# Optimization experiments

Hardware: AMD Instinct MI355X
Metric: run time of the kernel (lower is better)

## Reference

```python
import jax, jax.numpy as jnp
import numpy as np

N_ROWS = 8192
INPUT_DIM = 4096
EMBED_DIM = INPUT_DIM // 4
OUTPUT_DIM = 4096
NN = 16  # Taylor matrix size
RMS_EPS = 1.1920928955078125e-07  # torch fp32 finfo eps (F.rms_norm default)


def setup_inputs() -> dict:
    key = jax.random.key(0)
    ks = jax.random.split(key, 7)
    def lin(kw, fan_in, fan_out):
        bound = 1.0 / np.sqrt(fan_in)
        kw1, kw2 = jax.random.split(kw)
        W = jax.random.uniform(kw1, (fan_in, fan_out), jnp.float32, -bound, bound)
        b = jax.random.uniform(kw2, (fan_out,), jnp.float32, -bound, bound)
        return W, b
    x = jax.random.normal(ks[0], (N_ROWS, INPUT_DIM), jnp.float32)
    W_u, b_u = lin(ks[1], INPUT_DIM, EMBED_DIM)
    W_t, b_t = lin(ks[2], EMBED_DIM, NN * NN)
    W_s, b_s = lin(ks[3], NN * NN, OUTPUT_DIM)
    return {"x": x, "W_u": W_u, "b_u": b_u, "W_t": W_t, "b_t": b_t,
            "W_s": W_s, "b_s": b_s}


def _taylor_expm(M):
    # res = I + sum_{k=1}^{15} M^k / k!   (sequential, matches torch loop)
    B = M.shape[0]
    eye = jnp.broadcast_to(jnp.eye(NN, dtype=M.dtype), (B, NN, NN))
    def step(carry, k):
        term, res = carry
        term = jnp.einsum('bij,bjk->bik', term, M) / k
        return (term, res + term), None
    ks = jnp.arange(1, NN, dtype=M.dtype)
    (_, res), _ = jax.lax.scan(step, (eye, eye), ks)
    return res


def reference(x, W_u, b_u, W_t, b_t, W_s, b_s):
    # RMS norm (no learned scale)
    ms = jnp.mean(jnp.square(x), axis=-1, keepdims=True)
    xn = x * jax.lax.rsqrt(ms + RMS_EPS)
    latent = xn @ W_u + b_u                     # [N, embed]
    flat_m = latent @ W_t + b_t                 # [N, 256]
    mask = jnp.triu(jnp.ones((NN, NN), x.dtype), k=1).reshape(-1)
    flat_m = flat_m * mask
    m = flat_m.reshape(-1, NN, NN)              # [N, 16, 16] strictly upper
    exp_m = _taylor_expm(m)
    flat_exp = exp_m.reshape(x.shape[0], -1)    # [N, 256]
    return flat_exp @ W_s + b_s                 # [N, output_dim]
```

## Files before the change

### kernel.cpp

```cpp
#include <hip/hip_runtime.h>
#include <stdint.h>

typedef unsigned short u16;
typedef unsigned int u32;

using bf16x8 = __attribute__((ext_vector_type(8))) short;
using f32x4  = __attribute__((ext_vector_type(4))) float;

__device__ __forceinline__ float bf2f(u16 u) {
  union { u32 u; float f; } v; v.u = ((u32)u) << 16; return v.f;
}
__device__ __forceinline__ u16 f2bf(float f) {
  union { float f; u32 u; } v; v.f = f;
  u32 r = v.u + 0x7fffu + ((v.u >> 16) & 1u);
  return (u16)(r >> 16);
}
__device__ __forceinline__ short f2bf_s(float f) { return (short)f2bf(f); }

__global__ __launch_bounds__(256) void transpose_f32_bf16(
    const float* __restrict__ in, u16* __restrict__ out, int R, int C) {
  __shared__ u16 tile[32][33];
  const int tx = threadIdx.x, ty = threadIdx.y;
  const int icol = blockIdx.x * 32 + tx;
  const int irow0 = blockIdx.y * 32;
  #pragma unroll
  for (int i = ty; i < 32; i += 8)
    tile[i][tx] = f2bf(in[(size_t)(irow0 + i) * C + icol]);
  __syncthreads();
  const int ocol = blockIdx.y * 32 + tx;
  const int orow0 = blockIdx.x * 32;
  #pragma unroll
  for (int i = ty; i < 32; i += 8)
    out[(size_t)(orow0 + i) * R + ocol] = tile[tx][i];
}

__global__ __launch_bounds__(256) void rms_convert(
    const float* __restrict__ x, float* __restrict__ s, u16* __restrict__ xb, int K) {
  const int row = blockIdx.x;
  const float4* p = (const float4*)(x + (size_t)row * K);
  ushort4* q = (ushort4*)(xb + (size_t)row * K);
  float sum = 0.f;
  const int nvec = K >> 2;
  for (int i = threadIdx.x; i < nvec; i += 256) {
    float4 v = p[i];
    sum += v.x * v.x + v.y * v.y + v.z * v.z + v.w * v.w;
    ushort4 o;
    o.x = f2bf(v.x); o.y = f2bf(v.y); o.z = f2bf(v.z); o.w = f2bf(v.w);
    q[i] = o;
  }
  #pragma unroll
  for (int off = 32; off > 0; off >>= 1) sum += __shfl_down(sum, off, 64);
  __shared__ float part[4];
  if ((threadIdx.x & 63) == 0) part[threadIdx.x >> 6] = sum;
  __syncthreads();
  if (threadIdx.x == 0) {
    float tot = part[0] + part[1] + part[2] + part[3];
    s[row] = rsqrtf(tot / (float)K + 1.1920928955078125e-07f);
  }
}

template <int EPI, bool OUTF32>
__global__ __launch_bounds__(256) void gemm_bt(
    const u16* __restrict__ A, const u16* __restrict__ BT,
    const float* __restrict__ bias, const float* __restrict__ rowscale,
    void* __restrict__ Cv, int M, int N, int K) {
  __shared__ u16 As[128 * 32];
  __shared__ u16 Bs[128 * 32];
  const int t = threadIdx.x;
  const int lane = t & 63;
  const int w = t >> 6;
  const int wm = (w >> 1) * 64;
  const int wn = (w & 1) * 64;
  const int quad = lane >> 4;
  const int lrow = lane & 15;
  const int m0 = blockIdx.y * 128;
  const int n0 = blockIdx.x * 128;

  f32x4 acc[4][4] = {};

  const int srow = t >> 2;
  const int scol = (t & 3) * 8;
  const size_t abase = (size_t)(m0 + srow) * K + scol;
  const size_t bbase = (size_t)(n0 + srow) * K + scol;
  u16* const as_lo = As + srow * 32 + scol;
  u16* const as_hi = As + (64 + srow) * 32 + scol;
  u16* const bs_lo = Bs + srow * 32 + scol;
  u16* const bs_hi = Bs + (64 + srow) * 32 + scol;

  for (int k0 = 0; k0 < K; k0 += 32) {
    const bf16x8 ra0 = *(const bf16x8*)(A + abase + k0);
    const bf16x8 ra1 = *(const bf16x8*)(A + abase + (size_t)64 * K + k0);
    const bf16x8 rb0 = *(const bf16x8*)(BT + bbase + k0);
    const bf16x8 rb1 = *(const bf16x8*)(BT + bbase + (size_t)64 * K + k0);
    __syncthreads();
    *(bf16x8*)as_lo = ra0;
    *(bf16x8*)as_hi = ra1;
    *(bf16x8*)bs_lo = rb0;
    *(bf16x8*)bs_hi = rb1;
    __syncthreads();

    bf16x8 af[4], bv[4];
    #pragma unroll
    for (int i = 0; i < 4; ++i)
      af[i] = *(const bf16x8*)(As + (wm + i * 16 + lrow) * 32 + quad * 8);
    #pragma unroll
    for (int j = 0; j < 4; ++j)
      bv[j] = *(const bf16x8*)(Bs + (wn + j * 16 + lrow) * 32 + quad * 8);
    #pragma unroll
    for (int i = 0; i < 4; ++i)
      #pragma unroll
      for (int j = 0; j < 4; ++j)
        acc[i][j] = __builtin_amdgcn_mfma_f32_16x16x32_bf16(af[i], bv[j], acc[i][j], 0, 0, 0);
  }

  #pragma unroll
  for (int i = 0; i < 4; ++i) {
    const int row0 = m0 + wm + i * 16 + quad * 4;
    float sc[4];
    if (EPI == 0) {
      #pragma unroll
      for (int r = 0; r < 4; ++r) sc[r] = rowscale[row0 + r];
    }
    #pragma unroll
    for (int j = 0; j < 4; ++j) {
      const int col = n0 + wn + j * 16 + lrow;
      const float bvs = bias[col];
      #pragma unroll
      for (int r = 0; r < 4; ++r) {
        float v = acc[i][j][r];
        if (EPI == 0) v = v * sc[r] + bvs;
        else v += bvs;
        if (EPI == 1) {
          const int cc = col & 255;
          if ((cc & 15) <= (cc >> 4)) v = 0.f;
        }
        const size_t idx = (size_t)(row0 + r) * N + col;
        if (OUTF32) ((float*)Cv)[idx] = v;
        else        ((u16*)Cv)[idx] = f2bf(v);
      }
    }
  }
}

__global__ __launch_bounds__(256) void expm_taylor(
    const u16* __restrict__ Mi, u16* __restrict__ Eo) {
  __shared__ u16 mbuf[4][256];
  __shared__ float stage[2][4][16][17];
  const int t = threadIdx.x;
  const int w = t >> 6;
  const int lane = t & 63;
  const int q = lane >> 4;
  const int c = lane & 15;
  const size_t row = (size_t)blockIdx.x * 4 + w;

  *(uint2*)&mbuf[w][lane * 4] = *(const uint2*)(Mi + row * 256 + lane * 4);
  __syncthreads();

  const u16* mb = mbuf[w];
  const bf16x8 z8 = {0, 0, 0, 0, 0, 0, 0, 0};
  bf16x8 afrM = z8;
  bf16x8 bfr  = z8;
  if (q < 2) {
    #pragma unroll
    for (int jj = 0; jj < 8; ++jj) {
      afrM[jj] = (short)mb[c * 16 + q * 8 + jj];
      bfr[jj]  = (short)mb[(q * 8 + jj) * 16 + c];
    }
  }
  float res[4];
  #pragma unroll
  for (int r = 0; r < 4; ++r) {
    const int rw = q * 4 + r;
    res[r] = (rw == c ? 1.f : 0.f) + bf2f(mb[rw * 16 + c]);
  }

  for (int k = 2; k <= 15; ++k) {
    const f32x4 z = {0.f, 0.f, 0.f, 0.f};
    f32x4 P = __builtin_amdgcn_mfma_f32_16x16x32_bf16(afrM, bfr, z, 0, 0, 0);
    const float inv = 1.0f / (float)k;
    float tv[4];
    #pragma unroll
    for (int r = 0; r < 4; ++r) { tv[r] = P[r] * inv; res[r] += tv[r]; }
    if (k < 15) {
      #pragma unroll
      for (int r = 0; r < 4; ++r) stage[k & 1][w][q * 4 + r][c] = tv[r];
      __syncthreads();
      bfr = z8;
      if (q < 2) {
        #pragma unroll
        for (int jj = 0; jj < 8; ++jj) bfr[jj] = f2bf_s(stage[k & 1][w][q * 8 + jj][c]);
      }
    }
  }
  #pragma unroll
  for (int r = 0; r < 4; ++r)
    Eo[row * 256 + (size_t)(q * 4 + r) * 16 + c] = f2bf(res[r]);
}

extern "C" void kernel_launch(void* const* d_in, const int* in_sizes, int n_in,
                              void* d_out, int out_size, void* d_ws, size_t ws_size,
                              hipStream_t stream) {
  (void)in_sizes; (void)n_in; (void)out_size; (void)ws_size;
  const float* x   = (const float*)d_in[0];
  const float* W_u = (const float*)d_in[1];
  const float* b_u = (const float*)d_in[2];
  const float* W_t = (const float*)d_in[3];
  const float* b_t = (const float*)d_in[4];
  const float* W_s = (const float*)d_in[5];
  const float* b_s = (const float*)d_in[6];
  float* out = (float*)d_out;

  u16* xb     = (u16*)d_out;
  u16* latent = xb + (size_t)8192 * 4096;
  u16* mmat   = latent + (size_t)8192 * 1024;

  char* ws = (char*)d_ws;
  size_t off = 0;
  float* sscale = (float*)(ws + off); off += (size_t)8192 * sizeof(float);
  u16* WuT  = (u16*)(ws + off); off += (size_t)1024 * 4096 * 2;
  u16* WtT  = (u16*)(ws + off); off += (size_t)256 * 1024 * 2;
  u16* WsT  = (u16*)(ws + off); off += (size_t)4096 * 256 * 2;
  u16* eexp = (u16*)(ws + off); off += (size_t)8192 * 256 * 2;

  const dim3 tb(32, 8);
  transpose_f32_bf16<<<dim3(1024 / 32, 4096 / 32), tb, 0, stream>>>(W_u, WuT, 4096, 1024);
  transpose_f32_bf16<<<dim3(256 / 32, 1024 / 32), tb, 0, stream>>>(W_t, WtT, 1024, 256);
  transpose_f32_bf16<<<dim3(4096 / 32, 256 / 32), tb, 0, stream>>>(W_s, WsT, 256, 4096);

  rms_convert<<<8192, 256, 0, stream>>>(x, sscale, xb, 4096);

  gemm_bt<0, false><<<dim3(1024 / 128, 8192 / 128), 256, 0, stream>>>(
      xb, WuT, b_u, sscale, latent, 8192, 1024, 4096);
  gemm_bt<1, false><<<dim3(256 / 128, 8192 / 128), 256, 0, stream>>>(
      latent, WtT, b_t, nullptr, mmat, 8192, 256, 1024);
  expm_taylor<<<8192 / 4, 256, 0, stream>>>(mmat, eexp);
  gemm_bt<2, true><<<dim3(4096 / 128, 8192 / 128), 256, 0, stream>>>(
      eexp, WsT, b_s, nullptr, out, 8192, 4096, 256);
}
```

Before: 435.6 us.

## Load GEMM tiles directly into LDS with global_load_lds and XOR swizzle

Replaces the register-staged global-to-LDS copy in the bf16 GEMM with direct global_load_lds DMA loads of 16 bytes per lane. Each thread fetches a permuted 8-element column group chosen so that the linear per-thread LDS placement ends up XOR-swizzled, and the fragment reads apply the matching swizzle to reduce LDS bank conflicts. The aim is to cut VGPR staging and instruction overhead in the main loop. There is still no double buffering, so global latency stays exposed between the barriers, and correctness depends on the intrinsic's per-lane LDS placement matching t*4.

```diff
diff --git a/kernel.cpp b/kernel.cpp
--- a/kernel.cpp
+++ b/kernel.cpp
@@ -6,6 +6,11 @@
 
 using bf16x8 = __attribute__((ext_vector_type(8))) short;
 using f32x4  = __attribute__((ext_vector_type(4))) float;
+
+#define GLOBAL_AS __attribute__((address_space(1)))
+#define LDS_AS    __attribute__((address_space(3)))
+
+#define SWZ(r) (((r) >> 1) & 3)
 
 __device__ __forceinline__ float bf2f(u16 u) {
   union { u32 u; float f; } v; v.u = ((u32)u) << 16; return v.f;
@@ -79,33 +84,30 @@
   f32x4 acc[4][4] = {};
 
   const int srow = t >> 2;
-  const int scol = (t & 3) * 8;
-  const size_t abase = (size_t)(m0 + srow) * K + scol;
-  const size_t bbase = (size_t)(n0 + srow) * K + scol;
-  u16* const as_lo = As + srow * 32 + scol;
-  u16* const as_hi = As + (64 + srow) * 32 + scol;
-  u16* const bs_lo = Bs + srow * 32 + scol;
-  u16* const bs_hi = Bs + (64 + srow) * 32 + scol;
+  const int sg   = (t & 3) ^ SWZ(srow);
+  const size_t abase = (size_t)(m0 + srow) * K + sg * 8;
+  const size_t bbase = (size_t)(n0 + srow) * K + sg * 8;
 
   for (int k0 = 0; k0 < K; k0 += 32) {
-    const bf16x8 ra0 = *(const bf16x8*)(A + abase + k0);
-    const bf16x8 ra1 = *(const bf16x8*)(A + abase + (size_t)64 * K + k0);
-    const bf16x8 rb0 = *(const bf16x8*)(BT + bbase + k0);
-    const bf16x8 rb1 = *(const bf16x8*)(BT + bbase + (size_t)64 * K + k0);
     __syncthreads();
-    *(bf16x8*)as_lo = ra0;
-    *(bf16x8*)as_hi = ra1;
-    *(bf16x8*)bs_lo = rb0;
-    *(bf16x8*)bs_hi = rb1;
+    #pragma unroll
+    for (int r = 0; r < 2; ++r) {
+      const u16* ga = A + abase + (size_t)r * 64 * K + k0;
+      const u16* gb = BT + bbase + (size_t)r * 64 * K + k0;
+      __builtin_amdgcn_global_load_lds((const GLOBAL_AS u32*)ga,
+          (LDS_AS u32*)((u32*)As + r * 1024 + t * 4), 16, 0, 0);
+      __builtin_amdgcn_global_load_lds((const GLOBAL_AS u32*)gb,
+          (LDS_AS u32*)((u32*)Bs + r * 1024 + t * 4), 16, 0, 0);
+    }
     __syncthreads();
 
     bf16x8 af[4], bv[4];
     #pragma unroll
     for (int i = 0; i < 4; ++i)
-      af[i] = *(const bf16x8*)(As + (wm + i * 16 + lrow) * 32 + quad * 8);
+      af[i] = *(const bf16x8*)(As + (wm + i * 16 + lrow) * 32 + (quad ^ SWZ(lrow)) * 8);
     #pragma unroll
     for (int j = 0; j < 4; ++j)
-      bv[j] = *(const bf16x8*)(Bs + (wn + j * 16 + lrow) * 32 + quad * 8);
+      bv[j] = *(const bf16x8*)(Bs + (wn + j * 16 + lrow) * 32 + (quad ^ SWZ(lrow)) * 8);
     #pragma unroll
     for (int i = 0; i < 4; ++i)
       #pragma unroll
```

Result: no change. 431.3 us (-1.0%).
